# Kernel tuning notes

Measured on AMD Instinct MI355X. Metric: run time of the kernel, lower is better.

## Reference

```python
import jax, jax.numpy as jnp
import numpy as np

B, S, D, M = 8, 4096, 1024, 32
W_SCALE = 0.03  # keep gate pre-activations in a sane range


def setup_inputs() -> dict:
    key = jax.random.key(0)
    ks = jax.random.split(key, 7)
    return {
        "x": jax.random.normal(ks[0], (B, S, D), dtype=jnp.float32),
        "Wr": jax.random.normal(ks[1], (D, M), dtype=jnp.float32) * W_SCALE,
        "br": jnp.zeros((M,), dtype=jnp.float32),
        "Ww": jax.random.normal(ks[2], (D, M), dtype=jnp.float32) * W_SCALE,
        "bw": jnp.zeros((M,), dtype=jnp.float32),
        "Wm": jax.random.normal(ks[3], (D, M), dtype=jnp.float32) * W_SCALE,
        "bm": jnp.zeros((M,), dtype=jnp.float32),
        "Wp": jax.random.normal(ks[4], (M, D), dtype=jnp.float32) * W_SCALE,
        "bp": jnp.zeros((D,), dtype=jnp.float32),
        "Wo": jax.random.normal(ks[5], (2 * D, D), dtype=jnp.float32) * W_SCALE,
        "bo": jnp.zeros((D,), dtype=jnp.float32),
    }


def _forward(x, Wr, br, Ww, bw, Wm, bm, Wp, bp, Wo, bo):
    Bd, Sd, Dd = x.shape
    Md = Wr.shape[1]
    # All input-only linears are state-independent: batch them as big GEMMs.
    read_w = jax.nn.sigmoid(jnp.einsum("bsd,dm->bsm", x, Wr) + br)   # [B,S,M]
    write_w = jax.nn.sigmoid(jnp.einsum("bsd,dm->bsm", x, Ww) + bw)  # [B,S,M]
    new_mem = jnp.einsum("bsd,dm->bsm", x, Wm) + bm                  # [B,S,M]
    # Split output_gate weight: cat([x_t, mv]) @ Wo == x_t @ Wo_x + mv @ Wo_m
    Wo_x, Wo_m = Wo[:Dd], Wo[Dd:]
    pre_x = jnp.einsum("bsd,de->bse", x, Wo_x) + bo                  # [B,S,D]

    def step(mem, inp):
        r, w, nm, px = inp  # [B,M],[B,M],[B,M],[B,D]
        mv = (r * mem) @ Wp + bp                 # memory_proj(read * state)
        fused = jnp.tanh(px + mv @ Wo_m)         # output_gate(cat([x_t, mv]))
        mem_new = jax.lax.stop_gradient((1.0 - w) * mem + w * nm)  # .detach()
        return mem_new, fused

    mem0 = jnp.zeros((Bd, Md), dtype=x.dtype)
    xs = (
        jnp.swapaxes(read_w, 0, 1),
        jnp.swapaxes(write_w, 0, 1),
        jnp.swapaxes(new_mem, 0, 1),
        jnp.swapaxes(pre_x, 0, 1),
    )
    _, outs = jax.lax.scan(step, mem0, xs)  # outs: [S,B,D]
    return jnp.swapaxes(outs, 0, 1)         # [B,S,D]


def reference(x, Wr, br, Ww, bw, Wm, bm, Wp, bp, Wo, bo):
    return _forward(x, Wr, br, Ww, bw, Wm, bm, Wp, bp, Wo, bo)
```

## Files before the change

kernel.cpp:

```cpp
#include <hip/hip_runtime.h>

typedef unsigned short u16;
typedef __bf16 bf16x8 __attribute__((ext_vector_type(8)));
typedef __bf16 bf16x2 __attribute__((ext_vector_type(2)));
typedef float f32x4 __attribute__((ext_vector_type(4)));

#define BS_TOT 32768
#define SS 4096
#define DD 1024
#define MM 32

__device__ __forceinline__ float bf2f(u16 u) {
    union { float f; unsigned int i; } c; c.i = ((unsigned int)u) << 16; return c.f;
}
__device__ __forceinline__ u16 f2bf(float f) {
    union { float f; unsigned int i; } c; c.f = f;
    unsigned int r = c.i + 0x7FFFu + ((c.i >> 16) & 1u);
    return (u16)(r >> 16);
}
__device__ __forceinline__ f32x4 mfma16(bf16x8 a, bf16x8 b, f32x4 c) {
    return __builtin_amdgcn_mfma_f32_16x16x32_bf16(a, b, c, 0, 0, 0);
}
__device__ __forceinline__ u16 cvt_in(const void* p, size_t i, int f32m) {
    return f32m ? f2bf(((const float*)p)[i]) : ((const u16*)p)[i];
}
__device__ __forceinline__ unsigned cvt2(float x, float y) {
    bf16x2 p; p[0] = (__bf16)x; p[1] = (__bf16)y;
    union { bf16x2 v; unsigned u; } c; c.v = p; return c.u;
}
__device__ __forceinline__ uint4 pack8c(float4 a, float4 b) {
    uint4 v;
    v.x = cvt2(a.x, a.y); v.y = cvt2(a.z, a.w);
    v.z = cvt2(b.x, b.y); v.w = cvt2(b.z, b.w);
    return v;
}
__device__ __forceinline__ void gload16(u16* l, const u16* g) {
    __builtin_amdgcn_global_load_lds(
        (const __attribute__((address_space(1))) unsigned int*)(g),
        (__attribute__((address_space(3))) unsigned int*)(l),
        16, 0, 0);
}
__device__ __forceinline__ unsigned u4get(const uint4& v, int idx) {
    return idx == 0 ? v.x : idx == 1 ? v.y : idx == 2 ? v.z : v.w;
}
__device__ __forceinline__ u16 elem16(const uint4& a, const uint4& b, int j) {
    unsigned w = (j < 8) ? u4get(a, j >> 1) : u4get(b, (j - 8) >> 1);
    return (u16)((j & 1) ? (w >> 16) : (w & 0xFFFFu));
}

__global__ __launch_bounds__(64) void zej_detect(const unsigned int* __restrict__ xw,
                                                 int* __restrict__ flag)
{
    int lane = threadIdx.x;
    int cnt = 0;
#pragma unroll
    for (int i = 0; i < 16; i++) {
        unsigned int w = xw[lane * 16 + i];
        unsigned int e = (w >> 7) & 0xFFu;
        cnt += (e >= 110u && e <= 135u) ? 1 : 0;
    }
#pragma unroll
    for (int off = 32; off > 0; off >>= 1) cnt += __shfl_down(cnt, off);
    if (lane == 0) *flag = (cnt < 512) ? 1 : 0;
}

__global__ __launch_bounds__(256) void zej_pack(
    const void* __restrict__ Wr, const void* __restrict__ Ww, const void* __restrict__ Wm,
    const void* __restrict__ br, const void* __restrict__ bw, const void* __restrict__ bm,
    u16* __restrict__ W3T, u16* __restrict__ biasp, const int* __restrict__ flag)
{
    const int f32m = *flag;
    int i = blockIdx.x * 256 + threadIdx.x;
    if (i < 98304) {
        int j = i >> 10, k = i & 1023;
        W3T[i] = (j < 32) ? cvt_in(Wr, (size_t)k * 32 + j, f32m)
               : (j < 64) ? cvt_in(Ww, (size_t)k * 32 + (j - 32), f32m)
                          : cvt_in(Wm, (size_t)k * 32 + (j - 64), f32m);
        return;
    }
    i -= 98304;
    if (i < 96) {
        biasp[i] = (i < 32) ? cvt_in(br, i, f32m)
                 : (i < 64) ? cvt_in(bw, i - 32, f32m)
                            : cvt_in(bm, i - 64, f32m);
    }
}

__global__ __launch_bounds__(256) void zej_packT(
    const void* __restrict__ Wo, u16* __restrict__ WoxT, const int* __restrict__ flag)
{
    __shared__ float tile[64][65];
    const int f32m = *flag;
    const int t = threadIdx.x;
    const int kb = blockIdx.x & 15, nb = blockIdx.x >> 4;
    const int k0 = kb * 64, n0 = nb * 64;
#pragma unroll
    for (int i = 0; i < 16; i++) {
        int idx = i * 256 + t;
        int r = idx >> 6, c = idx & 63;
        size_t gi = (size_t)(k0 + r) * 1024 + n0 + c;
        tile[r][c] = f32m ? ((const float*)Wo)[gi] : bf2f(((const u16*)Wo)[gi]);
    }
    __syncthreads();
#pragma unroll
    for (int i = 0; i < 16; i++) {
        int idx = i * 256 + t;
        int nn = idx >> 6, kk = idx & 63;
        WoxT[(size_t)(n0 + nn) * 1024 + k0 + kk] = f2bf(tile[kk][nn]);
    }
}

__global__ __launch_bounds__(256) void zej_wpm_a(
    const void* __restrict__ Wp, const void* __restrict__ Wo,
    const void* __restrict__ bp,
    float* __restrict__ part, const int* __restrict__ flag)
{
    __shared__ float wpc[64 * 33];
    __shared__ float bpc[64];
    const int f32m = *flag;
    const int t = threadIdx.x;
    const int nb = blockIdx.x & 15;
    const int kb = blockIdx.x >> 4;
    const int d0 = kb * 64;

    for (int i = t; i < 2048; i += 256) {
        int m = i >> 6, dd = i & 63;
        float v = f32m ? ((const float*)Wp)[m * 1024 + d0 + dd]
                       : bf2f(((const u16*)Wp)[m * 1024 + d0 + dd]);
        wpc[dd * 33 + m] = v;
    }
    if (t < 64)
        bpc[t] = f32m ? ((const float*)bp)[d0 + t] : bf2f(((const u16*)bp)[d0 + t]);
    __syncthreads();

    const int n = nb * 64 + (t & 63);
    const int g = t >> 6;
    float acc[8];
#pragma unroll
    for (int j = 0; j < 8; j++) acc[j] = 0.f;
    float bacc = 0.f;

    for (int dd = 0; dd < 64; dd++) {
        float w = f32m ? ((const float*)Wo)[(size_t)(1024 + d0 + dd) * 1024 + n]
                       : bf2f(((const u16*)Wo)[(size_t)(1024 + d0 + dd) * 1024 + n]);
        const float* wp8 = &wpc[dd * 33 + g * 8];
#pragma unroll
        for (int j = 0; j < 8; j++) acc[j] += wp8[j] * w;
        if (g == 0) bacc += bpc[dd] * w;
    }
    float* pk = part + (size_t)kb * 33792;
#pragma unroll
    for (int j = 0; j < 8; j++) pk[(g * 8 + j) * 1024 + n] = acc[j];
    if (g == 0) pk[32 * 1024 + n] = bacc;
}

__global__ __launch_bounds__(256) void zej_wpm_b(
    const float* __restrict__ part, const void* __restrict__ bo,
    u16* __restrict__ WpmT, float* __restrict__ bpm, const int* __restrict__ flag)
{
    const int f32m = *flag;
    const int t = threadIdx.x;
    const int bid = blockIdx.x;
    if (bid < 128) {
        int m = bid >> 2;
        int n = (bid & 3) * 256 + t;
        float acc = 0.f;
#pragma unroll
        for (int kb = 0; kb < 16; kb++) acc += part[(size_t)kb * 33792 + m * 1024 + n];
        WpmT[(size_t)n * 32 + m] = f2bf(acc);
    } else {
        int n = (bid - 128) * 256 + t;
        float acc = 0.f;
#pragma unroll
        for (int kb = 0; kb < 16; kb++) acc += part[(size_t)kb * 33792 + 32 * 1024 + n];
        float b = f32m ? ((const float*)bo)[n] : bf2f(((const u16*)bo)[n]);
        bpm[n] = acc + b;
    }
}

__global__ __launch_bounds__(256) void zej_gates(
    const void* __restrict__ x, const u16* __restrict__ W3T,
    const u16* __restrict__ biasp, u16* __restrict__ gtc,
    u16* __restrict__ xb, const int* __restrict__ flag)
{
    __shared__ __align__(16) u16 As[128][88];
    __shared__ __align__(16) u16 Bs[96][88];
    const int f32m = *flag;
    const int t = threadIdx.x;
    const int lane = t & 63;
    const int wv = t >> 6;
    const int row0 = blockIdx.x * 128;
    const int lm = lane & 15, lq = lane >> 4;

    f32x4 acc[2][6];
    f32x4 z = {0.f, 0.f, 0.f, 0.f};
#pragma unroll
    for (int i = 0; i < 2; i++)
#pragma unroll
        for (int j = 0; j < 6; j++) acc[i][j] = z;

    for (int k0 = 0; k0 < 1024; k0 += 64) {
#pragma unroll
        for (int c = 0; c < 4; c++) {
            int chunk = t + c * 256;
            int r = chunk >> 3, kc = (chunk & 7) * 8;
            size_t gi = (size_t)(row0 + r) * 1024 + k0 + kc;
            uint4 v;
            if (f32m) {
                const float* xf = (const float*)x;
                float4 f0 = *(const float4*)(xf + gi);
                float4 f1 = *(const float4*)(xf + gi + 4);
                v = pack8c(f0, f1);
            } else {
                v = *(const uint4*)((const u16*)x + gi);
            }
            *(uint4*)&As[r][kc] = v;
            *(uint4*)(xb + gi) = v;
        }
#pragma unroll
        for (int c = 0; c < 3; c++) {
            int chunk = t + c * 256;
            int j = chunk >> 3, kc = (chunk & 7) * 8;
            *(uint4*)&Bs[j][kc] = *(const uint4*)&W3T[j * 1024 + k0 + kc];
        }
        __syncthreads();
#pragma unroll
        for (int ks = 0; ks < 2; ks++) {
            int kk = ks * 32 + lq * 8;
            bf16x8 a[2], b[6];
#pragma unroll
            for (int rt = 0; rt < 2; rt++) a[rt] = *(const bf16x8*)&As[wv * 32 + rt * 16 + lm][kk];
#pragma unroll
            for (int ct = 0; ct < 6; ct++) b[ct] = *(const bf16x8*)&Bs[ct * 16 + lm][kk];
#pragma unroll
            for (int rt = 0; rt < 2; rt++)
#pragma unroll
                for (int ct = 0; ct < 6; ct++)
                    acc[rt][ct] = mfma16(a[rt], b[ct], acc[rt][ct]);
        }
        __syncthreads();
    }
#pragma unroll
    for (int rt = 0; rt < 2; rt++) {
#pragma unroll
        for (int ct = 0; ct < 6; ct++) {
            int col = ct * 16 + lm;
            float bias = bf2f(biasp[col]);
            bool sig = (col < 64);
#pragma unroll
            for (int p = 0; p < 4; p++) {
                int R = row0 + wv * 32 + rt * 16 + lq * 4 + p;
                float v = acc[rt][ct][p] + bias;
                if (sig) v = 1.f / (1.f + __expf(-v));
                gtc[(size_t)col * BS_TOT + R] = f2bf(v);
            }
        }
    }
}

__global__ __launch_bounds__(256) void zej_scan(
    const u16* __restrict__ gtc, u16* __restrict__ rmc)
{
    __shared__ float sA[4], sB[4];
    const int c = blockIdx.x;
    const int b = c >> 5;
    const int m = c & 31;
    const int t = threadIdx.x;
    const int lane = t & 63;
    const int wv = t >> 6;
    const size_t base = (size_t)b * SS;
    const u16* gr  = gtc + (size_t)( 0 + m) * BS_TOT + base;
    const u16* gw  = gtc + (size_t)(32 + m) * BS_TOT + base;
    const u16* gnm = gtc + (size_t)(64 + m) * BS_TOT + base;
    const int i0 = t * 16;

    uint4 w0 = *(const uint4*)(gw + i0);
    uint4 w1 = *(const uint4*)(gw + i0 + 8);
    uint4 n0 = *(const uint4*)(gnm + i0);
    uint4 n1 = *(const uint4*)(gnm + i0 + 8);

    float A = 1.f, Bc = 0.f;
#pragma unroll
    for (int j = 0; j < 16; j++) {
        float w  = bf2f(elem16(w0, w1, j));
        float nm = bf2f(elem16(n0, n1, j));
        float a = 1.f - w;
        Bc = a * Bc + w * nm;
        A *= a;
    }
    float Ai = A, Bi = Bc;
    for (int off = 1; off < 64; off <<= 1) {
        float Ap = __shfl_up(Ai, off);
        float Bp = __shfl_up(Bi, off);
        if (lane >= off) { Bi = Ai * Bp + Bi; Ai = Ai * Ap; }
    }
    if (lane == 63) { sA[wv] = Ai; sB[wv] = Bi; }
    __syncthreads();
    float Aw = 1.f, Bw = 0.f;
    for (int k = 0; k < wv; k++) {
        float a2 = sA[k];
        Bw = a2 * Bw + sB[k];
        Aw = Aw * a2;
    }
    float Ae = __shfl_up(Ai, 1);
    float Be = __shfl_up(Bi, 1);
    if (lane == 0) { Ae = 1.f; Be = 0.f; }
    float mem = Ae * Bw + Be;

    uint4 r0 = *(const uint4*)(gr + i0);
    uint4 r1 = *(const uint4*)(gr + i0 + 8);
    u16 o[16];
#pragma unroll
    for (int j = 0; j < 16; j++) {
        float r  = bf2f(elem16(r0, r1, j));
        float w  = bf2f(elem16(w0, w1, j));
        float nm = bf2f(elem16(n0, n1, j));
        o[j] = f2bf(r * mem);
        mem = (1.f - w) * mem + w * nm;
    }
    u16* dst = rmc + (size_t)m * BS_TOT + base + i0;
    *(uint4*)dst       = *(uint4*)&o[0];
    *(uint4*)(dst + 8) = *(uint4*)&o[8];
}

__global__ __launch_bounds__(256) void zej_rmt(
    const u16* __restrict__ rmc, u16* __restrict__ rm)
{
    __shared__ __align__(16) u16 tile[32][136];
    const int t = threadIdx.x;
    const int R0 = blockIdx.x * 128;
#pragma unroll
    for (int c = 0; c < 2; c++) {
        int idx = t + c * 256;
        int m = idx >> 4, kq = (idx & 15) * 8;
        *(uint4*)&tile[m][kq] = *(const uint4*)&rmc[(size_t)m * BS_TOT + R0 + kq];
    }
    __syncthreads();
#pragma unroll
    for (int c = 0; c < 2; c++) {
        int idx = t + c * 256;
        int r = idx & 127, mq = (idx >> 7) * 8;
        u16 tmp[8];
#pragma unroll
        for (int j = 0; j < 8; j++) tmp[j] = tile[mq + j][r];
        *(uint4*)&rm[(size_t)(R0 + r) * 32 + mq] = *(uint4*)tmp;
    }
}

__global__ __launch_bounds__(256) void zej_out(
    const u16* __restrict__ xb, const u16* __restrict__ rm,
    const u16* __restrict__ WoxT, const u16* __restrict__ WpmT,
    const float* __restrict__ bpm, float* __restrict__ out)
{
    __shared__ __align__(16) u16 As[128 * 64];
    __shared__ __align__(16) u16 Bs[128 * 64];
    const int t = threadIdx.x;
    const int lane = t & 63;
    const int wv = t >> 6;
    const int wr = (wv >> 1) * 64;
    const int wc = (wv & 1) * 64;
    const int bid = blockIdx.x;
    const int lin = (bid & 7) * 256 + (bid >> 3);
    const int row0 = (lin >> 3) * 128;
    const int n0 = (lin & 7) * 128;
    const int lm = lane & 15, lq = lane >> 4;

    f32x4 acc[4][4];
    f32x4 z = {0.f, 0.f, 0.f, 0.f};
#pragma unroll
    for (int i = 0; i < 4; i++)
#pragma unroll
        for (int j = 0; j < 4; j++) acc[i][j] = z;

    const int sr = lane >> 3;
    const int slot = lane & 7;
    const int kcs = 8 * (slot ^ sr);

    for (int k0 = 0; k0 < 1024; k0 += 64) {
#pragma unroll
        for (int i = 0; i < 4; i++) {
            int ra = (wv * 4 + i) * 8 + sr;
            gload16(&As[(wv * 4 + i) * 512], xb   + (size_t)(row0 + ra) * 1024 + k0 + kcs);
            gload16(&Bs[(wv * 4 + i) * 512], WoxT + (size_t)(n0  + ra) * 1024 + k0 + kcs);
        }
        __syncthreads();
#pragma unroll
        for (int ks = 0; ks < 2; ks++) {
            bf16x8 a[4], b[4];
#pragma unroll
            for (int rt = 0; rt < 4; rt++) {
                int R = wr + rt * 16 + lm;
                int cb = (ks * 64 + lq * 16) ^ ((R & 7) << 4);
                a[rt] = *(const bf16x8*)((const char*)As + R * 128 + cb);
            }
#pragma unroll
            for (int ct = 0; ct < 4; ct++) {
                int R = wc + ct * 16 + lm;
                int cb = (ks * 64 + lq * 16) ^ ((R & 7) << 4);
                b[ct] = *(const bf16x8*)((const char*)Bs + R * 128 + cb);
            }
#pragma unroll
            for (int rt = 0; rt < 4; rt++)
#pragma unroll
                for (int ct = 0; ct < 4; ct++)
                    acc[rt][ct] = mfma16(a[rt], b[ct], acc[rt][ct]);
        }
        __syncthreads();
    }

    {
        const int sr2 = lane >> 2;
        const int slot2 = lane & 3;
        const int kcs2 = 8 * (slot2 ^ (sr2 & 3));
#pragma unroll
        for (int i = 0; i < 2; i++) {
            int ra = (wv * 2 + i) * 16 + sr2;
            gload16(&As[(wv * 2 + i) * 512], rm   + (size_t)(row0 + ra) * 32 + kcs2);
            gload16(&Bs[(wv * 2 + i) * 512], WpmT + (size_t)(n0  + ra) * 32 + kcs2);
        }
        __syncthreads();
        bf16x8 a[4], b[4];
#pragma unroll
        for (int rt = 0; rt < 4; rt++) {
            int R = wr + rt * 16 + lm;
            a[rt] = *(const bf16x8*)((const char*)As + R * 64 + ((lq * 16) ^ ((R & 3) << 4)));
        }
#pragma unroll
        for (int ct = 0; ct < 4; ct++) {
            int R = wc + ct * 16 + lm;
            b[ct] = *(const bf16x8*)((const char*)Bs + R * 64 + ((lq * 16) ^ ((R & 3) << 4)));
        }
#pragma unroll
        for (int rt = 0; rt < 4; rt++)
#pragma unroll
            for (int ct = 0; ct < 4; ct++)
                acc[rt][ct] = mfma16(a[rt], b[ct], acc[rt][ct]);
    }

#pragma unroll
    for (int rt = 0; rt < 4; rt++) {
#pragma unroll
        for (int ct = 0; ct < 4; ct++) {
            int n = n0 + wc + ct * 16 + lm;
            float bias = bpm[n];
#pragma unroll
            for (int p = 0; p < 4; p++) {
                int R = row0 + wr + rt * 16 + lq * 4 + p;
                float v = acc[rt][ct][p] + bias;
                float e = __expf(2.f * v);
                out[(size_t)R * 1024 + n] = 1.f - 2.f / (e + 1.f);
            }
        }
    }
}

extern "C" void kernel_launch(void* const* d_in, const int* in_sizes, int n_in,
                              void* d_out, int out_size, void* d_ws, size_t ws_size,
                              hipStream_t stream)
{
    const void* x  = d_in[0];
    const void* Wr = d_in[1];
    const void* br = d_in[2];
    const void* Ww = d_in[3];
    const void* bw = d_in[4];
    const void* Wm = d_in[5];
    const void* bm = d_in[6];
    const void* Wp = d_in[7];
    const void* bp = d_in[8];
    const void* Wo = d_in[9];
    const void* bo = d_in[10];
    float* out = (float*)d_out;

    char* ws = (char*)d_ws;
    int* flag   = (int*)ws;
    u16* W3T    = (u16*)(ws + 1024);
    u16* WoxT   = (u16*)(ws + 197632);
    u16* WpmT   = (u16*)(ws + 2294784);
    u16* biasp  = (u16*)(ws + 2360320);
    float* bpm  = (float*)(ws + 2361344);
    u16* gtc    = (u16*)(ws + 2365440);
    u16* rmc    = (u16*)(ws + 8656896);
    u16* rm     = (u16*)(ws + 10754048);
    u16* xb     = (u16*)(ws + 12851200);
    float* Wpm_part = (float*)(ws + 2365440);

    zej_detect<<<1, 64, 0, stream>>>((const unsigned int*)x, flag);
    zej_pack<<<385, 256, 0, stream>>>(Wr, Ww, Wm, br, bw, bm, W3T, biasp, flag);
    zej_packT<<<256, 256, 0, stream>>>(Wo, WoxT, flag);
    zej_wpm_a<<<256, 256, 0, stream>>>(Wp, Wo, bp, Wpm_part, flag);
    zej_wpm_b<<<132, 256, 0, stream>>>(Wpm_part, bo, WpmT, bpm, flag);
    zej_gates<<<BS_TOT / 128, 256, 0, stream>>>(x, W3T, biasp, gtc, xb, flag);
    zej_scan<<<256, 256, 0, stream>>>(gtc, rmc);
    zej_rmt<<<256, 256, 0, stream>>>(rmc, rm);
    zej_out<<<2048, 256, 0, stream>>>(xb, rm, WoxT, WpmT, bpm, out);
}
```

Measured before the change: 409.2 us.

## Fuse prep kernels, drop rm transpose, retile gates, vectorize output stores

Merges the dtype-detect, weight-pack, Wo transpose and Wpm partial-product kernels into a single launch that detects dtype per block. The Wpm reduction moves into the gates launch as extra blocks. Gates now use 64-row tiles and stage results through shared memory for coalesced column-major stores. The separate rm transpose kernel is removed: the output GEMM reads the column-major scan result directly into LDS and gathers it. Operand order is swapped so the output epilogue writes float4 rows. This cuts launch count and global round trips, at the cost of redundant per-block detection and a strided LDS gather.

Measured after the change: 403.5 us. About the same (-1.4%).

```diff
diff --git a/kernel.cpp b/kernel.cpp
--- a/kernel.cpp
+++ b/kernel.cpp
@@ -48,160 +48,162 @@
     return (u16)((j & 1) ? (w >> 16) : (w & 0xFFFFu));
 }
 
-__global__ __launch_bounds__(64) void zej_detect(const unsigned int* __restrict__ xw,
-                                                 int* __restrict__ flag)
-{
-    int lane = threadIdx.x;
+__device__ __forceinline__ int block_detect_f32(const unsigned int* xw) {
+    __shared__ int s_cnt;
+    if (threadIdx.x == 0) s_cnt = 0;
+    __syncthreads();
     int cnt = 0;
 #pragma unroll
-    for (int i = 0; i < 16; i++) {
-        unsigned int w = xw[lane * 16 + i];
+    for (int i = 0; i < 4; i++) {
+        unsigned int w = xw[threadIdx.x * 4 + i];
         unsigned int e = (w >> 7) & 0xFFu;
         cnt += (e >= 110u && e <= 135u) ? 1 : 0;
     }
 #pragma unroll
     for (int off = 32; off > 0; off >>= 1) cnt += __shfl_down(cnt, off);
-    if (lane == 0) *flag = (cnt < 512) ? 1 : 0;
-}
-
-__global__ __launch_bounds__(256) void zej_pack(
+    if ((threadIdx.x & 63) == 0) atomicAdd(&s_cnt, cnt);
+    __syncthreads();
+    return (s_cnt < 512) ? 1 : 0;
+}
+
+__global__ __launch_bounds__(256) void zej_prep(
+    const void* __restrict__ x,
     const void* __restrict__ Wr, const void* __restrict__ Ww, const void* __restrict__ Wm,
+    const void* __restrict__ Wp, const void* __restrict__ Wo,
     const void* __restrict__ br, const void* __restrict__ bw, const void* __restrict__ bm,
-    u16* __restrict__ W3T, u16* __restrict__ biasp, const int* __restrict__ flag)
-{
-    const int f32m = *flag;
-    int i = blockIdx.x * 256 + threadIdx.x;
-    if (i < 98304) {
-        int j = i >> 10, k = i & 1023;
-        W3T[i] = (j < 32) ? cvt_in(Wr, (size_t)k * 32 + j, f32m)
-               : (j < 64) ? cvt_in(Ww, (size_t)k * 32 + (j - 32), f32m)
-                          : cvt_in(Wm, (size_t)k * 32 + (j - 64), f32m);
-        return;
-    }
-    i -= 98304;
-    if (i < 96) {
-        biasp[i] = (i < 32) ? cvt_in(br, i, f32m)
-                 : (i < 64) ? cvt_in(bw, i - 32, f32m)
-                            : cvt_in(bm, i - 64, f32m);
-    }
-}
-
-__global__ __launch_bounds__(256) void zej_packT(
-    const void* __restrict__ Wo, u16* __restrict__ WoxT, const int* __restrict__ flag)
+    const void* __restrict__ bp,
+    u16* __restrict__ W3T, u16* __restrict__ WoxT, u16* __restrict__ biasp,
+    float* __restrict__ part)
 {
     __shared__ float tile[64][65];
-    const int f32m = *flag;
-    const int t = threadIdx.x;
-    const int kb = blockIdx.x & 15, nb = blockIdx.x >> 4;
-    const int k0 = kb * 64, n0 = nb * 64;
-#pragma unroll
-    for (int i = 0; i < 16; i++) {
-        int idx = i * 256 + t;
-        int r = idx >> 6, c = idx & 63;
-        size_t gi = (size_t)(k0 + r) * 1024 + n0 + c;
-        tile[r][c] = f32m ? ((const float*)Wo)[gi] : bf2f(((const u16*)Wo)[gi]);
-    }
-    __syncthreads();
-#pragma unroll
-    for (int i = 0; i < 16; i++) {
-        int idx = i * 256 + t;
-        int nn = idx >> 6, kk = idx & 63;
-        WoxT[(size_t)(n0 + nn) * 1024 + k0 + kk] = f2bf(tile[kk][nn]);
-    }
-}
-
-__global__ __launch_bounds__(256) void zej_wpm_a(
-    const void* __restrict__ Wp, const void* __restrict__ Wo,
-    const void* __restrict__ bp,
-    float* __restrict__ part, const int* __restrict__ flag)
-{
-    __shared__ float wpc[64 * 33];
-    __shared__ float bpc[64];
-    const int f32m = *flag;
-    const int t = threadIdx.x;
-    const int nb = blockIdx.x & 15;
-    const int kb = blockIdx.x >> 4;
-    const int d0 = kb * 64;
-
-    for (int i = t; i < 2048; i += 256) {
-        int m = i >> 6, dd = i & 63;
-        float v = f32m ? ((const float*)Wp)[m * 1024 + d0 + dd]
-                       : bf2f(((const u16*)Wp)[m * 1024 + d0 + dd]);
-        wpc[dd * 33 + m] = v;
-    }
-    if (t < 64)
-        bpc[t] = f32m ? ((const float*)bp)[d0 + t] : bf2f(((const u16*)bp)[d0 + t]);
-    __syncthreads();
-
-    const int n = nb * 64 + (t & 63);
-    const int g = t >> 6;
-    float acc[8];
-#pragma unroll
-    for (int j = 0; j < 8; j++) acc[j] = 0.f;
-    float bacc = 0.f;
-
-    for (int dd = 0; dd < 64; dd++) {
-        float w = f32m ? ((const float*)Wo)[(size_t)(1024 + d0 + dd) * 1024 + n]
-                       : bf2f(((const u16*)Wo)[(size_t)(1024 + d0 + dd) * 1024 + n]);
-        const float* wp8 = &wpc[dd * 33 + g * 8];
-#pragma unroll
-        for (int j = 0; j < 8; j++) acc[j] += wp8[j] * w;
-        if (g == 0) bacc += bpc[dd] * w;
-    }
-    float* pk = part + (size_t)kb * 33792;
-#pragma unroll
-    for (int j = 0; j < 8; j++) pk[(g * 8 + j) * 1024 + n] = acc[j];
-    if (g == 0) pk[32 * 1024 + n] = bacc;
-}
-
-__global__ __launch_bounds__(256) void zej_wpm_b(
-    const float* __restrict__ part, const void* __restrict__ bo,
-    u16* __restrict__ WpmT, float* __restrict__ bpm, const int* __restrict__ flag)
-{
-    const int f32m = *flag;
+    __shared__ float wpc[128 * 33];
+    __shared__ float bpc[128];
+    const int f32m = block_detect_f32((const unsigned int*)x);
     const int t = threadIdx.x;
     const int bid = blockIdx.x;
-    if (bid < 128) {
-        int m = bid >> 2;
-        int n = (bid & 3) * 256 + t;
-        float acc = 0.f;
-#pragma unroll
-        for (int kb = 0; kb < 16; kb++) acc += part[(size_t)kb * 33792 + m * 1024 + n];
-        WpmT[(size_t)n * 32 + m] = f2bf(acc);
-    } else {
-        int n = (bid - 128) * 256 + t;
-        float acc = 0.f;
-#pragma unroll
-        for (int kb = 0; kb < 16; kb++) acc += part[(size_t)kb * 33792 + 32 * 1024 + n];
-        float b = f32m ? ((const float*)bo)[n] : bf2f(((const u16*)bo)[n]);
-        bpm[n] = acc + b;
+
+    if (bid < 385) {
+        int i = bid * 256 + t;
+        if (i < 98304) {
+            int j = i >> 10, k = i & 1023;
+            W3T[i] = (j < 32) ? cvt_in(Wr, (size_t)k * 32 + j, f32m)
+                   : (j < 64) ? cvt_in(Ww, (size_t)k * 32 + (j - 32), f32m)
+                              : cvt_in(Wm, (size_t)k * 32 + (j - 64), f32m);
+            return;
+        }
+        i -= 98304;
+        if (i < 96) {
+            biasp[i] = (i < 32) ? cvt_in(br, i, f32m)
+                     : (i < 64) ? cvt_in(bw, i - 32, f32m)
+                                : cvt_in(bm, i - 64, f32m);
+        }
+        return;
+    }
+    if (bid < 641) {
+        int b2 = bid - 385;
+        const int kb = b2 & 15, nb = b2 >> 4;
+        const int k0 = kb * 64, n0 = nb * 64;
+#pragma unroll
+        for (int i = 0; i < 16; i++) {
+            int idx = i * 256 + t;
+            int r = idx >> 6, c = idx & 63;
+            size_t gi = (size_t)(k0 + r) * 1024 + n0 + c;
+            tile[r][c] = f32m ? ((const float*)Wo)[gi] : bf2f(((const u16*)Wo)[gi]);
+        }
+        __syncthreads();
+#pragma unroll
+        for (int i = 0; i < 16; i++) {
+            int idx = i * 256 + t;
+            int nn = idx >> 6, kk = idx & 63;
+            WoxT[(size_t)(n0 + nn) * 1024 + k0 + kk] = f2bf(tile[kk][nn]);
+        }
+        return;
+    }
+    {
+        int b2 = bid - 641;
+        const int nb = b2 & 15;
+        const int kb = b2 >> 4;
+        const int d0 = kb * 128;
+
+        for (int i = t; i < 4096; i += 256) {
+            int m = i >> 7, dd = i & 127;
+            float v = f32m ? ((const float*)Wp)[m * 1024 + d0 + dd]
+                           : bf2f(((const u16*)Wp)[m * 1024 + d0 + dd]);
+            wpc[dd * 33 + m] = v;
+        }
+        if (t < 128)
+            bpc[t] = f32m ? ((const float*)bp)[d0 + t] : bf2f(((const u16*)bp)[d0 + t]);
+        __syncthreads();
+
+        const int n = nb * 64 + (t & 63);
+        const int g = t >> 6;
+        float acc[8];
+#pragma unroll
+        for (int j = 0; j < 8; j++) acc[j] = 0.f;
+        float bacc = 0.f;
+
+        for (int dd = 0; dd < 128; dd++) {
+            float w = f32m ? ((const float*)Wo)[(size_t)(1024 + d0 + dd) * 1024 + n]
+                           : bf2f(((const u16*)Wo)[(size_t)(1024 + d0 + dd) * 1024 + n]);
+            const float* wp8 = &wpc[dd * 33 + g * 8];
+#pragma unroll
+            for (int j = 0; j < 8; j++) acc[j] += wp8[j] * w;
+            if (g == 0) bacc += bpc[dd] * w;
+        }
+        float* pk = part + (size_t)kb * 33792;
+#pragma unroll
+        for (int j = 0; j < 8; j++) pk[(g * 8 + j) * 1024 + n] = acc[j];
+        if (g == 0) pk[32 * 1024 + n] = bacc;
     }
 }
 
 __global__ __launch_bounds__(256) void zej_gates(
     const void* __restrict__ x, const u16* __restrict__ W3T,
-    const u16* __restrict__ biasp, u16* __restrict__ gtc,
-    u16* __restrict__ xb, const int* __restrict__ flag)
+    const u16* __restrict__ biasp,
+    const float* __restrict__ part, const void* __restrict__ bo,
+    u16* __restrict__ gtc, u16* __restrict__ xb,
+    u16* __restrict__ WpmT, float* __restrict__ bpm)
 {
-    __shared__ __align__(16) u16 As[128][88];
+    __shared__ __align__(16) u16 As[64][88];
     __shared__ __align__(16) u16 Bs[96][88];
-    const int f32m = *flag;
+    __shared__ __align__(16) u16 Ts[96][72];
+    const int f32m = block_detect_f32((const unsigned int*)x);
     const int t = threadIdx.x;
+    const int bid = blockIdx.x;
+
+    if (bid >= 512) {
+        int b2 = bid - 512;
+        if (b2 < 128) {
+            int m = b2 >> 2;
+            int n = (b2 & 3) * 256 + t;
+            float acc = 0.f;
+#pragma unroll
+            for (int kb = 0; kb < 8; kb++) acc += part[(size_t)kb * 33792 + m * 1024 + n];
+            WpmT[(size_t)n * 32 + m] = f2bf(acc);
+        } else {
+            int n = (b2 - 128) * 256 + t;
+            float acc = 0.f;
+#pragma unroll
+            for (int kb = 0; kb < 8; kb++) acc += part[(size_t)kb * 33792 + 32 * 1024 + n];
+            float b = f32m ? ((const float*)bo)[n] : bf2f(((const u16*)bo)[n]);
+            bpm[n] = acc + b;
+        }
+        return;
+    }
+
     const int lane = t & 63;
     const int wv = t >> 6;
-    const int row0 = blockIdx.x * 128;
+    const int row0 = bid * 64;
     const int lm = lane & 15, lq = lane >> 4;
 
-    f32x4 acc[2][6];
+    f32x4 acc[6];
     f32x4 z = {0.f, 0.f, 0.f, 0.f};
 #pragma unroll
-    for (int i = 0; i < 2; i++)
-#pragma unroll
-        for (int j = 0; j < 6; j++) acc[i][j] = z;
+    for (int j = 0; j < 6; j++) acc[j] = z;
 
     for (int k0 = 0; k0 < 1024; k0 += 64) {
 #pragma unroll
-        for (int c = 0; c < 4; c++) {
+        for (int c = 0; c < 2; c++) {
             int chunk = t + c * 256;
             int r = chunk >> 3, kc = (chunk & 7) * 8;
             size_t gi = (size_t)(row0 + r) * 1024 + k0 + kc;
@@ -227,34 +229,34 @@
 #pragma unroll
         for (int ks = 0; ks < 2; ks++) {
             int kk = ks * 32 + lq * 8;
-            bf16x8 a[2], b[6];
-#pragma unroll
-            for (int rt = 0; rt < 2; rt++) a[rt] = *(const bf16x8*)&As[wv * 32 + rt * 16 + lm][kk];
-#pragma unroll
-            for (int ct = 0; ct < 6; ct++) b[ct] = *(const bf16x8*)&Bs[ct * 16 + lm][kk];
-#pragma unroll
-            for (int rt = 0; rt < 2; rt++)
-#pragma unroll
-                for (int ct = 0; ct < 6; ct++)
-                    acc[rt][ct] = mfma16(a[rt], b[ct], acc[rt][ct]);
-        }
-        __syncthreads();
-    }
-#pragma unroll
-    for (int rt = 0; rt < 2; rt++) {
-#pragma unroll
-        for (int ct = 0; ct < 6; ct++) {
-            int col = ct * 16 + lm;
-            float bias = bf2f(biasp[col]);
-            bool sig = (col < 64);
-#pragma unroll
-            for (int p = 0; p < 4; p++) {
-                int R = row0 + wv * 32 + rt * 16 + lq * 4 + p;
-                float v = acc[rt][ct][p] + bias;
-                if (sig) v = 1.f / (1.f + __expf(-v));
-                gtc[(size_t)col * BS_TOT + R] = f2bf(v);
-            }
-        }
+            bf16x8 a = *(const bf16x8*)&As[wv * 16 + lm][kk];
+#pragma unroll
+            for (int ct = 0; ct < 6; ct++) {
+                bf16x8 b = *(const bf16x8*)&Bs[ct * 16 + lm][kk];
+                acc[ct] = mfma16(a, b, acc[ct]);
+            }
+        }
+        __syncthreads();
+    }
+#pragma unroll
+    for (int ct = 0; ct < 6; ct++) {
+        int col = ct * 16 + lm;
+        float bias = bf2f(biasp[col]);
+        bool sig = (col < 64);
+#pragma unroll
+        for (int p = 0; p < 4; p++) {
+            int lr = wv * 16 + lq * 4 + p;
+            float v = acc[ct][p] + bias;
+            if (sig) v = 1.f / (1.f + __expf(-v));
+            Ts[col][lr] = f2bf(v);
+        }
+    }
+    __syncthreads();
+#pragma unroll
+    for (int c = 0; c < 3; c++) {
+        int chunk = t + c * 256;
+        int col = chunk >> 3, off = (chunk & 7) * 8;
+        *(uint4*)&gtc[(size_t)col * BS_TOT + row0 + off] = *(uint4*)&Ts[col][off];
     }
 }
 
@@ -296,11 +298,10 @@
     }
     if (lane == 63) { sA[wv] = Ai; sB[wv] = Bi; }
     __syncthreads();
-    float Aw = 1.f, Bw = 0.f;
+    float Bw = 0.f;
     for (int k = 0; k < wv; k++) {
         float a2 = sA[k];
         Bw = a2 * Bw + sB[k];
-        Aw = Aw * a2;
     }
     float Ae = __shfl_up(Ai, 1);
     float Be = __shfl_up(Bi, 1);
@@ -323,32 +324,8 @@
     *(uint4*)(dst + 8) = *(uint4*)&o[8];
 }
 
-__global__ __launch_bounds__(256) void zej_rmt(
-    const u16* __restrict__ rmc, u16* __restrict__ rm)
-{
-    __shared__ __align__(16) u16 tile[32][136];
-    const int t = threadIdx.x;
-    const int R0 = blockIdx.x * 128;
-#pragma unroll
-    for (int c = 0; c < 2; c++) {
-        int idx = t + c * 256;
-        int m = idx >> 4, kq = (idx & 15) * 8;
-        *(uint4*)&tile[m][kq] = *(const uint4*)&rmc[(size_t)m * BS_TOT + R0 + kq];
-    }
-    __syncthreads();
-#pragma unroll
-    for (int c = 0; c < 2; c++) {
-        int idx = t + c * 256;
-        int r = idx & 127, mq = (idx >> 7) * 8;
-        u16 tmp[8];
-#pragma unroll
-        for (int j = 0; j < 8; j++) tmp[j] = tile[mq + j][r];
-        *(uint4*)&rm[(size_t)(R0 + r) * 32 + mq] = *(uint4*)tmp;
-    }
-}
-
 __global__ __launch_bounds__(256) void zej_out(
-    const u16* __restrict__ xb, const u16* __restrict__ rm,
+    const u16* __restrict__ xb, const u16* __restrict__ rmc,
     const u16* __restrict__ WoxT, const u16* __restrict__ WpmT,
     const float* __restrict__ bpm, float* __restrict__ out)
 {
@@ -403,27 +380,35 @@
             for (int rt = 0; rt < 4; rt++)
 #pragma unroll
                 for (int ct = 0; ct < 4; ct++)
-                    acc[rt][ct] = mfma16(a[rt], b[ct], acc[rt][ct]);
+                    acc[rt][ct] = mfma16(b[ct], a[rt], acc[rt][ct]);
         }
         __syncthreads();
     }
 
     {
+        u16* Rs = (u16*)As;
+#pragma unroll
+        for (int c = 0; c < 2; c++) {
+            int chunk = t + c * 256;
+            int m = chunk >> 4, kq = (chunk & 15) * 8;
+            *(uint4*)&Rs[m * 136 + kq] = *(const uint4*)&rmc[(size_t)m * BS_TOT + row0 + kq];
+        }
         const int sr2 = lane >> 2;
         const int slot2 = lane & 3;
         const int kcs2 = 8 * (slot2 ^ (sr2 & 3));
 #pragma unroll
         for (int i = 0; i < 2; i++) {
             int ra = (wv * 2 + i) * 16 + sr2;
-            gload16(&As[(wv * 2 + i) * 512], rm   + (size_t)(row0 + ra) * 32 + kcs2);
-            gload16(&Bs[(wv * 2 + i) * 512], WpmT + (size_t)(n0  + ra) * 32 + kcs2);
+            gload16(&Bs[(wv * 2 + i) * 512], WpmT + (size_t)(n0 + ra) * 32 + kcs2);
         }
         __syncthreads();
         bf16x8 a[4], b[4];
 #pragma unroll
         for (int rt = 0; rt < 4; rt++) {
             int R = wr + rt * 16 + lm;
-            a[rt] = *(const bf16x8*)((const char*)As + R * 64 + ((lq * 16) ^ ((R & 3) << 4)));
+#pragma unroll
+            for (int j = 0; j < 8; j++)
+                ((u16*)&a[rt])[j] = Rs[(lq * 8 + j) * 136 + R];
         }
 #pragma unroll
         for (int ct = 0; ct < 4; ct++) {
@@ -434,22 +419,34 @@
         for (int rt = 0; rt < 4; rt++)
 #pragma unroll
             for (int ct = 0; ct < 4; ct++)
-                acc[rt][ct] = mfma16(a[rt], b[ct], acc[rt][ct]);
+                acc[rt][ct] = mfma16(b[ct], a[rt], acc[rt][ct]);
     }
 
 #pragma unroll
     for (int rt = 0; rt < 4; rt++) {
 #pragma unroll
         for (int ct = 0; ct < 4; ct++) {
-            int n = n0 + wc + ct * 16 + lm;
-            float bias = bpm[n];
-#pragma unroll
-            for (int p = 0; p < 4; p++) {
-                int R = row0 + wr + rt * 16 + lq * 4 + p;
-                float v = acc[rt][ct][p] + bias;
-                float e = __expf(2.f * v);
-                out[(size_t)R * 1024 + n] = 1.f - 2.f / (e + 1.f);
-            }
+            int R = row0 + wr + rt * 16 + lm;
+            int nb4 = n0 + wc + ct * 16 + lq * 4;
+            float4 bias = *(const float4*)&bpm[nb4];
+            float4 o;
+            {
+                float v = acc[rt][ct][0] + bias.x;
+                float e = __expf(2.f * v); o.x = 1.f - 2.f / (e + 1.f);
+            }
+            {
+                float v = acc[rt][ct][1] + bias.y;
+                float e = __expf(2.f * v); o.y = 1.f - 2.f / (e + 1.f);
+            }
+            {
+                float v = acc[rt][ct][2] + bias.z;
+                float e = __expf(2.f * v); o.z = 1.f - 2.f / (e + 1.f);
+            }
+            {
+                float v = acc[rt][ct][3] + bias.w;
+                float e = __expf(2.f * v); o.w = 1.f - 2.f / (e + 1.f);
+            }
+            *(float4*)&out[(size_t)R * 1024 + nb4] = o;
         }
     }
 }
@@ -472,25 +469,20 @@
     float* out = (float*)d_out;
 
     char* ws = (char*)d_ws;
-    int* flag   = (int*)ws;
-    u16* W3T    = (u16*)(ws + 1024);
-    u16* WoxT   = (u16*)(ws + 197632);
-    u16* WpmT   = (u16*)(ws + 2294784);
-    u16* biasp  = (u16*)(ws + 2360320);
-    float* bpm  = (float*)(ws + 2361344);
-    u16* gtc    = (u16*)(ws + 2365440);
-    u16* rmc    = (u16*)(ws + 8656896);
-    u16* rm     = (u16*)(ws + 10754048);
-    u16* xb     = (u16*)(ws + 12851200);
-    float* Wpm_part = (float*)(ws + 2365440);
-
-    zej_detect<<<1, 64, 0, stream>>>((const unsigned int*)x, flag);
-    zej_pack<<<385, 256, 0, stream>>>(Wr, Ww, Wm, br, bw, bm, W3T, biasp, flag);
-    zej_packT<<<256, 256, 0, stream>>>(Wo, WoxT, flag);
-    zej_wpm_a<<<256, 256, 0, stream>>>(Wp, Wo, bp, Wpm_part, flag);
-    zej_wpm_b<<<132, 256, 0, stream>>>(Wpm_part, bo, WpmT, bpm, flag);
-    zej_gates<<<BS_TOT / 128, 256, 0, stream>>>(x, W3T, biasp, gtc, xb, flag);
+    u16* W3T    = (u16*)(ws + 0);
+    u16* WoxT   = (u16*)(ws + 196608);
+    u16* WpmT   = (u16*)(ws + 2293760);
+    u16* biasp  = (u16*)(ws + 2359296);
+    float* bpm  = (float*)(ws + 2360320);
+    u16* gtc    = (u16*)(ws + 2364416);
+    u16* rmc    = (u16*)(ws + 8655872);
+    u16* xb     = (u16*)(ws + 10753024);
+    float* Wpm_part = (float*)(ws + 8655872);
+
+    zej_prep<<<769, 256, 0, stream>>>(x, Wr, Ww, Wm, Wp, Wo, br, bw, bm, bp,
+                                      W3T, WoxT, biasp, Wpm_part);
+    zej_gates<<<644, 256, 0, stream>>>(x, W3T, biasp, Wpm_part, bo,
+                                       gtc, xb, WpmT, bpm);
     zej_scan<<<256, 256, 0, stream>>>(gtc, rmc);
-    zej_rmt<<<256, 256, 0, stream>>>(rmc, rm);
-    zej_out<<<2048, 256, 0, stream>>>(xb, rm, WoxT, WpmT, bpm, out);
-}
+    zej_out<<<2048, 256, 0, stream>>>(xb, rmc, WoxT, WpmT, bpm, out);
+}
```
